# Performance work log

Measured on AMD Instinct MI355X. Metric: run time of the kernel, lower is better.

## Reference

```python
import jax, jax.numpy as jnp
import numpy as np

N = 50000      # nodes
E = 800000     # edges (before self-loops)
F_IN = 128     # raw node feature dim
D = 500        # GCN_in_dim = gcn_dim = h_mlp_dim
T = 200000     # number of triplets


def setup_inputs() -> dict:
    key = jax.random.key(0)
    ks = jax.random.split(key, 13)
    s = 0.05
    return {
        "feats": jax.random.normal(ks[0], (N, F_IN), jnp.float32),
        "W_aff": jax.random.normal(ks[1], (F_IN, D), jnp.float32) * s,
        "b_aff": jax.random.normal(ks[2], (D,), jnp.float32) * s,
        "W_gcn": jax.random.normal(ks[3], (D, D), jnp.float32) * s,
        "b_gcn": jax.random.normal(ks[4], (D,), jnp.float32) * s,
        "W_pred_in": jax.random.normal(ks[5], (2 * D, D), jnp.float32) * s,
        "b_pred_in": jax.random.normal(ks[6], (D,), jnp.float32) * s,
        "W_pred_out": jax.random.normal(ks[7], (D, 1), jnp.float32) * s,
        "b_pred_out": jax.random.normal(ks[8], (1,), jnp.float32) * s,
        "src": jax.random.randint(ks[9], (E,), 0, N),
        "dst": jax.random.randint(ks[10], (E,), 0, N),
        "triplets": jax.random.randint(ks[11], (T, 3), 0, N),
    }


def reference(feats, W_aff, b_aff, W_gcn, b_gcn, W_pred_in, b_pred_in,
              W_pred_out, b_pred_out, src, dst, triplets):
    n = feats.shape[0]
    # LinearAffine (use_pre_linearAffine=True)
    x = feats @ W_aff + b_aff                      # [N, D]

    # dgl.add_self_loop
    loop = jnp.arange(n)
    s_idx = jnp.concatenate([src, loop])
    d_idx = jnp.concatenate([dst, loop])

    # GraphConv, norm='both', no edge weights, activation=None
    ones = jnp.ones(s_idx.shape[0], jnp.float32)
    out_deg = jax.ops.segment_sum(ones, s_idx, num_segments=n)
    in_deg = jax.ops.segment_sum(ones, d_idx, num_segments=n)
    norm_src = jnp.where(out_deg > 0, jax.lax.rsqrt(out_deg), 0.0)  # [N]
    norm_dst = jnp.where(in_deg > 0, jax.lax.rsqrt(in_deg), 0.0)    # [N]

    xw = x @ W_gcn                                  # [N, D]
    msg = xw[s_idx] * norm_src[s_idx, None]         # [E+N, D] gather
    agg = jax.ops.segment_sum(msg, d_idx, num_segments=n)  # scatter-add
    embedding = agg * norm_dst[:, None] + b_gcn     # [N, D]

    # triplet gather + MLP_edge_predictor (layer_num=2: cat->Linear->Linear)
    s_feat = embedding[triplets[:, 0]]              # [T, D]
    o_feat = embedding[triplets[:, 2]]              # [T, D]
    t = jnp.concatenate([s_feat, o_feat], axis=-1) @ W_pred_in + b_pred_in
    weights = t @ W_pred_out + b_pred_out           # [T, 1]
    return (weights, embedding)
```

## Files before the change

### kernel.cpp

```cpp
#include <hip/hip_runtime.h>


typedef float f32x4 __attribute__((ext_vector_type(4)));
typedef short s16x8 __attribute__((ext_vector_type(8)));

__device__ __forceinline__ unsigned short f2bf(float f) {
    unsigned u = __float_as_uint(f);
    unsigned r = (u + 0x7FFFu + ((u >> 16) & 1u)) >> 16;
    return (unsigned short)r;
}

__device__ __forceinline__ void async_ld16(const void* g, void* lds) {
    __builtin_amdgcn_global_load_lds(
        (const __attribute__((address_space(1))) unsigned int*)g,
        (__attribute__((address_space(3))) unsigned int*)lds,
        16, 0, 0);
}

__global__ __launch_bounds__(256) void init_kernel(
    float* __restrict__ u, int nU4, unsigned* __restrict__ gpad, int nG,
    float* __restrict__ hpad, int nH, int* __restrict__ bh, int nB) {
    const int stride = gridDim.x * blockDim.x;
    const int i0 = blockIdx.x * blockDim.x + threadIdx.x;
    for (int i = i0; i < nU4; i += stride)
        *reinterpret_cast<float4*>(u + i * 4) = make_float4(0.f, 0.f, 0.f, 0.f);
    for (int i = i0; i < nG; i += stride) gpad[i] = 0u;
    for (int i = i0; i < nH; i += stride) hpad[i] = 0.f;
    for (int i = i0; i < nB; i += stride) bh[i] = 0;
}

__global__ __launch_bounds__(256) void hist2_kernel(
    const int* __restrict__ src, const int* __restrict__ dst,
    int* __restrict__ bhist_src, int* __restrict__ bhist_dst, int E) {
    __shared__ int lhs[256], lhd[256];
    lhs[threadIdx.x] = 0;
    lhd[threadIdx.x] = 0;
    __syncthreads();
    const int stride = gridDim.x * blockDim.x;
    for (int e = blockIdx.x * blockDim.x + threadIdx.x; e < E; e += stride) {
        atomicAdd(&lhs[src[e] >> 8], 1);
        atomicAdd(&lhd[dst[e] >> 8], 1);
    }
    __syncthreads();
    int cs = lhs[threadIdx.x], cd = lhd[threadIdx.x];
    if (cs > 0) atomicAdd(&bhist_src[threadIdx.x], cs);
    if (cd > 0) atomicAdd(&bhist_dst[threadIdx.x], cd);
}

__global__ void bscan2_kernel(const int* __restrict__ bhist_src, const int* __restrict__ bhist_dst,
                              int* __restrict__ sbbase, int* __restrict__ sbcursor,
                              int* __restrict__ dbbase, int* __restrict__ dbcursor,
                              int nbuk, int E) {
    __shared__ int sv[256];
    const int tid = threadIdx.x;

    int c = (tid < nbuk) ? bhist_src[tid] : 0;
    sv[tid] = c;
    __syncthreads();
    for (int st = 1; st < 256; st <<= 1) {
        int t = (tid >= st) ? sv[tid - st] : 0;
        __syncthreads();
        sv[tid] += t;
        __syncthreads();
    }
    if (tid < nbuk) { int ex = sv[tid] - c; sbbase[tid] = ex; sbcursor[tid] = ex; }
    if (tid == 0) sbbase[nbuk] = E;
    __syncthreads();

    c = (tid < nbuk) ? bhist_dst[tid] : 0;
    sv[tid] = c;
    __syncthreads();
    for (int st = 1; st < 256; st <<= 1) {
        int t = (tid >= st) ? sv[tid - st] : 0;
        __syncthreads();
        sv[tid] += t;
        __syncthreads();
    }
    if (tid < nbuk) { int ex = sv[tid] - c; dbbase[tid] = ex; dbcursor[tid] = ex; }
    if (tid == 0) dbbase[nbuk] = E;
}

#define PCH 4096
__global__ __launch_bounds__(256) void fused_partition_kernel(
    const int* __restrict__ src, const int* __restrict__ dst,
    int* __restrict__ dcursor, unsigned long long* __restrict__ pairs,
    int* __restrict__ scursor, int* __restrict__ ssorted,
    int E, int nbuk) {
    __shared__ int lhist[256];
    __shared__ int lbase[256];
    __shared__ int gbase[256];
    __shared__ int scanv[256];
    __shared__ unsigned long long lpair[PCH];
    __shared__ unsigned char lbid[PCH];

    const int tid = threadIdx.x;
    const int c0 = blockIdx.x * PCH;
    int cnt = E - c0; if (cnt > PCH) cnt = PCH;

    int dv[16], sv[16], rk[16];

    lhist[tid] = 0;
    __syncthreads();
#pragma unroll
    for (int q = 0; q < 16; ++q) {
        int e = c0 + q * 256 + tid;
        if (e < E) {
            int d = dst[e];
            dv[q] = d;
            sv[q] = src[e];
            rk[q] = atomicAdd(&lhist[d >> 8], 1);
        } else {
            dv[q] = -1;
            sv[q] = -1;
        }
    }
    __syncthreads();

    int c = lhist[tid];
    scanv[tid] = c;
    __syncthreads();
    for (int st = 1; st < 256; st <<= 1) {
        int t = (tid >= st) ? scanv[tid - st] : 0;
        __syncthreads();
        scanv[tid] += t;
        __syncthreads();
    }
    lbase[tid] = scanv[tid] - c;
    if (tid < nbuk && c > 0) gbase[tid] = atomicAdd(&dcursor[tid], c);
    __syncthreads();

#pragma unroll
    for (int q = 0; q < 16; ++q) {
        if (dv[q] >= 0) {
            int b = dv[q] >> 8;
            int slot = lbase[b] + rk[q];
            lpair[slot] = ((unsigned long long)(unsigned)dv[q] << 32) | (unsigned)sv[q];
            lbid[slot] = (unsigned char)b;
        }
    }
    __syncthreads();

    for (int i = tid; i < cnt; i += 256) {
        int b = lbid[i];
        pairs[(long)gbase[b] + (i - lbase[b])] = lpair[i];
    }
    __syncthreads();

    int* lval = (int*)lpair;
    lhist[tid] = 0;
    __syncthreads();
#pragma unroll
    for (int q = 0; q < 16; ++q) {
        if (sv[q] >= 0) rk[q] = atomicAdd(&lhist[sv[q] >> 8], 1);
    }
    __syncthreads();

    c = lhist[tid];
    scanv[tid] = c;
    __syncthreads();
    for (int st = 1; st < 256; st <<= 1) {
        int t = (tid >= st) ? scanv[tid - st] : 0;
        __syncthreads();
        scanv[tid] += t;
        __syncthreads();
    }
    lbase[tid] = scanv[tid] - c;
    if (tid < nbuk && c > 0) gbase[tid] = atomicAdd(&scursor[tid], c);
    __syncthreads();

#pragma unroll
    for (int q = 0; q < 16; ++q) {
        if (sv[q] >= 0) {
            int b = sv[q] >> 8;
            int slot = lbase[b] + rk[q];
            lval[slot] = sv[q];
            lbid[slot] = (unsigned char)b;
        }
    }
    __syncthreads();

    for (int i = tid; i < cnt; i += 256) {
        int b = lbid[i];
        ssorted[(long)gbase[b] + (i - lbase[b])] = lval[i];
    }
}

__global__ __launch_bounds__(256) void bucket_finalize_kernel(
    const unsigned long long* __restrict__ pairs, const int* __restrict__ dbbase,
    const int* __restrict__ ssorted, const int* __restrict__ sbbase,
    const float* __restrict__ feats,
    int* __restrict__ row_ptr, float* __restrict__ ndv,
    int* __restrict__ csr_src, float* __restrict__ ns,
    unsigned short* __restrict__ fs16, int N) {
    __shared__ int hist[256];
    __shared__ int scanv[256];
    __shared__ int lcur[256];
    __shared__ float nsv[256];
    const int tid = threadIdx.x;
    const int b = blockIdx.x;
    const int node = b * 256 + tid;

    const int e0 = dbbase[b], e1 = dbbase[b + 1];
    hist[tid] = 0;
    __syncthreads();
    for (int e = e0 + tid; e < e1; e += 256) {
        int d = (int)(pairs[e] >> 32);
        atomicAdd(&hist[d & 255], 1);
    }
    __syncthreads();

    int c = hist[tid];
    scanv[tid] = c;
    __syncthreads();
    for (int st = 1; st < 256; st <<= 1) {
        int t = (tid >= st) ? scanv[tid - st] : 0;
        __syncthreads();
        scanv[tid] += t;
        __syncthreads();
    }
    int excl = scanv[tid] - c;
    if (node < N) {
        row_ptr[node] = e0 + excl;
        ndv[node] = rsqrtf((float)(c + 1));
    }
    if (node == N) row_ptr[N] = e0 + excl;
    lcur[tid] = excl;
    __syncthreads();

    for (int e = e0 + tid; e < e1; e += 256) {
        unsigned long long pr = pairs[e];
        int d = (int)(pr >> 32);
        int r = atomicAdd(&lcur[d & 255], 1);
        csr_src[e0 + r] = (int)(pr & 0xFFFFFFFFu);
    }

    __syncthreads();
    hist[tid] = 0;
    __syncthreads();
    const int s0 = sbbase[b], s1 = sbbase[b + 1];
    for (int e = s0 + tid; e < s1; e += 256) atomicAdd(&hist[ssorted[e] & 255], 1);
    __syncthreads();
    float nsval = rsqrtf((float)(hist[tid] + 1));
    nsv[tid] = nsval;
    if (node < N) ns[node] = nsval;
    __syncthreads();

    for (int r0 = 0; r0 < 256; r0 += 16) {
        int r = r0 + (tid >> 4);
        int nn = b * 256 + r;
        if (nn >= N) break;
        int cq = (tid & 15) * 8;
        float s = nsv[r];
        const float* pf = feats + (long)nn * 128 + cq;
        float4 a = *reinterpret_cast<const float4*>(pf);
        float4 d2 = *reinterpret_cast<const float4*>(pf + 4);
        uint4 o;
        o.x = (unsigned)f2bf(a.x * s) | ((unsigned)f2bf(a.y * s) << 16);
        o.y = (unsigned)f2bf(a.z * s) | ((unsigned)f2bf(a.w * s) << 16);
        o.z = (unsigned)f2bf(d2.x * s) | ((unsigned)f2bf(d2.y * s) << 16);
        o.w = (unsigned)f2bf(d2.z * s) | ((unsigned)f2bf(d2.w * s) << 16);
        *reinterpret_cast<uint4*>(fs16 + (long)nn * 128 + cq) = o;
    }
}

__global__ __launch_bounds__(256) void prep1_kernel(
    const float* __restrict__ b_aff, const float* __restrict__ W_gcn,
    float* __restrict__ part,
    const float* __restrict__ Win, const float* __restrict__ wout,
    float* __restrict__ v,
    const float* __restrict__ b_in, const float* __restrict__ b_out,
    float* __restrict__ bdot,
    int D, int PD, int NBbc, int NBv, int nbper) {
    __shared__ float sm[256];
    const int b = blockIdx.x;
    const int tid = threadIdx.x;

    if (b < NBbc) {
        int nblk = b % nbper;
        int cch = b / nbper;
        int n = nblk * 256 + tid;
        if (n >= PD) return;
        float s = 0.f;
        if (n < D) {
            int k0 = cch * 8;
            int k1 = k0 + 8; if (k1 > D) k1 = D;
            for (int k = k0; k < k1; ++k) s = fmaf(b_aff[k], W_gcn[(long)k * D + n], s);
        }
        part[(long)cch * PD + n] = s;
    } else if (b < NBbc + NBv) {
        int k = (b - NBbc) * 4 + (tid >> 6);
        int lane = tid & 63;
        if (k >= 2 * D) return;
        float s = 0.f;
        for (int cc = lane; cc < D; cc += 64) s = fmaf(Win[(long)k * D + cc], wout[cc], s);
#pragma unroll
        for (int m = 32; m > 0; m >>= 1) s += __shfl_down(s, m);
        if (lane == 0) v[k] = s;
    } else {
        float s = 0.f;
        for (int cc = tid; cc < D; cc += 256) s = fmaf(b_in[cc], wout[cc], s);
        sm[tid] = s;
        __syncthreads();
        for (int st = 128; st > 0; st >>= 1) {
            if (tid < st) sm[tid] += sm[tid + st];
            __syncthreads();
        }
        if (tid == 0) bdot[0] = sm[0] + b_out[0];
    }
}

__global__ __launch_bounds__(256) void sgemm_kernel(const float* __restrict__ A, int lda,
                                                    const float* __restrict__ B, int ldb,
                                                    float* __restrict__ Cp, int ldc,
                                                    int M, int N, int K) {
    __shared__ __align__(16) float As[16][68];
    __shared__ __align__(16) float Bs[16][68];
    const int tid = threadIdx.x;
    const int tx = tid & 15, ty = tid >> 4;
    const int row0 = blockIdx.x * 64;
    const int col0 = blockIdx.y * 64;
    const int kbeg = blockIdx.z * 128;
    int kend = kbeg + 128; if (kend > K) kend = K;
    float* C = Cp + (long)blockIdx.z * M * ldc;

    const int a_row = tid >> 2;
    const int a_k   = (tid & 3) * 4;
    const int b_k   = tid >> 4;
    const int b_c   = (tid & 15) * 4;

    float acc[4][4] = {};

    for (int k0 = kbeg; k0 < kend; k0 += 16) {
        float4 av = make_float4(0.f, 0.f, 0.f, 0.f);
        {
            int gr = row0 + a_row;
            int gk = k0 + a_k;
            if (gr < M) {
                if (gk + 3 < kend) {
                    av = *reinterpret_cast<const float4*>(&A[(long)gr * lda + gk]);
                } else {
                    float t0 = (gk + 0 < kend) ? A[(long)gr * lda + gk + 0] : 0.f;
                    float t1 = (gk + 1 < kend) ? A[(long)gr * lda + gk + 1] : 0.f;
                    float t2 = (gk + 2 < kend) ? A[(long)gr * lda + gk + 2] : 0.f;
                    float t3 = (gk + 3 < kend) ? A[(long)gr * lda + gk + 3] : 0.f;
                    av = make_float4(t0, t1, t2, t3);
                }
            }
        }
        float4 bv = make_float4(0.f, 0.f, 0.f, 0.f);
        {
            int gk = k0 + b_k;
            int gc = col0 + b_c;
            if (gk < kend) {
                if (gc + 3 < N) {
                    bv = *reinterpret_cast<const float4*>(&B[(long)gk * ldb + gc]);
                } else {
                    float t0 = (gc + 0 < N) ? B[(long)gk * ldb + gc + 0] : 0.f;
                    float t1 = (gc + 1 < N) ? B[(long)gk * ldb + gc + 1] : 0.f;
                    float t2 = (gc + 2 < N) ? B[(long)gk * ldb + gc + 2] : 0.f;
                    float t3 = (gc + 3 < N) ? B[(long)gk * ldb + gc + 3] : 0.f;
                    bv = make_float4(t0, t1, t2, t3);
                }
            }
        }
        __syncthreads();
        As[a_k + 0][a_row] = av.x;
        As[a_k + 1][a_row] = av.y;
        As[a_k + 2][a_row] = av.z;
        As[a_k + 3][a_row] = av.w;
        *reinterpret_cast<float4*>(&Bs[b_k][b_c]) = bv;
        __syncthreads();

#pragma unroll
        for (int k = 0; k < 16; ++k) {
            const float4 a = *reinterpret_cast<const float4*>(&As[k][ty * 4]);
            const float4 b = *reinterpret_cast<const float4*>(&Bs[k][tx * 4]);
            const float avv[4] = {a.x, a.y, a.z, a.w};
            const float bvv[4] = {b.x, b.y, b.z, b.w};
#pragma unroll
            for (int i = 0; i < 4; ++i)
#pragma unroll
                for (int j = 0; j < 4; ++j)
                    acc[i][j] = fmaf(avv[i], bvv[j], acc[i][j]);
        }
    }

#pragma unroll
    for (int i = 0; i < 4; ++i) {
        int r = row0 + ty * 4 + i;
        if (r >= M) continue;
#pragma unroll
        for (int j = 0; j < 4; ++j) {
            int c = col0 + tx * 4 + j;
            if (c < N) C[(long)r * ldc + c] = acc[i][j];
        }
    }
}

__global__ __launch_bounds__(256) void convBt_pad_kernel(
    const float* __restrict__ Wcp, unsigned short* __restrict__ Bt,
    const float* __restrict__ part, const float* __restrict__ b_gcn,
    const float* __restrict__ v, float* __restrict__ bcp,
    float* __restrict__ bgp, float* __restrict__ v1p, float* __restrict__ v2p,
    int D, int PD, int NC, int F, int nConvBlk) {
    const int b = blockIdx.x;
    const int tid = threadIdx.x;
    if (b < nConvBlk) {
        int idx = b * 256 + tid;
        if (idx >= PD * 16) return;
        int n = idx >> 4;
        int k8 = (idx & 15) * 8;
        uint4 o = make_uint4(0, 0, 0, 0);
        if (n < D) {
            unsigned short t[8];
            const long FD = (long)F * D;
#pragma unroll
            for (int q = 0; q < 8; ++q) {
                long off = (long)(k8 + q) * D + n;
                float val = Wcp[off] + Wcp[FD + off] + Wcp[2 * FD + off] + Wcp[3 * FD + off];
                t[q] = f2bf(val);
            }
            o.x = (unsigned)t[0] | ((unsigned)t[1] << 16);
            o.y = (unsigned)t[2] | ((unsigned)t[3] << 16);
            o.z = (unsigned)t[4] | ((unsigned)t[5] << 16);
            o.w = (unsigned)t[6] | ((unsigned)t[7] << 16);
        }
        *reinterpret_cast<uint4*>(Bt + (long)n * 128 + k8) = o;
    } else {
        int i = (b - nConvBlk) * 256 + tid;
        if (i < PD) {
            float s = 0.f;
            for (int c = 0; c < NC; ++c) s += part[(long)c * PD + i];
            bcp[i] = s;
            bgp[i] = (i < D) ? b_gcn[i] : 0.f;
            v1p[i] = (i < D) ? v[i] : 0.f;
            v2p[i] = (i < D) ? v[D + i] : 0.f;
        }
    }
}

__global__ __launch_bounds__(256) void gather_feats_kernel(
    const unsigned short* __restrict__ fs16, const int* __restrict__ csr_src,
    const int* __restrict__ row_ptr, const float* __restrict__ ns,
    unsigned short* __restrict__ g16, float* __restrict__ h, int N) {
    int d = blockIdx.x * 4 + (threadIdx.x >> 6);
    int lane = threadIdx.x & 63;
    if (d >= N) return;
    const int g = lane >> 4;
    const int fl = lane & 15;

    float a[8] = {0.f, 0.f, 0.f, 0.f, 0.f, 0.f, 0.f, 0.f};
    float hacc = 0.f;

    const int beg = row_ptr[d], end = row_ptr[d + 1];
    for (int j0 = beg; j0 < end; j0 += 64) {
        int cnt = end - j0;
        if (cnt > 64) cnt = 64;
        int s = (lane < cnt) ? csr_src[j0 + lane] : 0;
        if (lane < cnt) hacc += ns[s];
        for (int k = 0; k < cnt; k += 8) {
            int k0 = k + g, k1 = k + 4 + g;
            int i0 = __shfl(s, k0 & 63);
            int i1 = __shfl(s, k1 & 63);
            uint4 v0 = make_uint4(0u, 0u, 0u, 0u), v1 = make_uint4(0u, 0u, 0u, 0u);
            if (k0 < cnt) v0 = *reinterpret_cast<const uint4*>(fs16 + (long)i0 * 128 + fl * 8);
            if (k1 < cnt) v1 = *reinterpret_cast<const uint4*>(fs16 + (long)i1 * 128 + fl * 8);
            a[0] += __uint_as_float(v0.x << 16); a[1] += __uint_as_float(v0.x & 0xFFFF0000u);
            a[2] += __uint_as_float(v0.y << 16); a[3] += __uint_as_float(v0.y & 0xFFFF0000u);
            a[4] += __uint_as_float(v0.z << 16); a[5] += __uint_as_float(v0.z & 0xFFFF0000u);
            a[6] += __uint_as_float(v0.w << 16); a[7] += __uint_as_float(v0.w & 0xFFFF0000u);
            a[0] += __uint_as_float(v1.x << 16); a[1] += __uint_as_float(v1.x & 0xFFFF0000u);
            a[2] += __uint_as_float(v1.y << 16); a[3] += __uint_as_float(v1.y & 0xFFFF0000u);
            a[4] += __uint_as_float(v1.z << 16); a[5] += __uint_as_float(v1.z & 0xFFFF0000u);
            a[6] += __uint_as_float(v1.w << 16); a[7] += __uint_as_float(v1.w & 0xFFFF0000u);
        }
    }

#pragma unroll
    for (int r = 0; r < 8; ++r) {
        a[r] += __shfl_xor(a[r], 16);
        a[r] += __shfl_xor(a[r], 32);
    }
    {
        uint4 sv4 = *reinterpret_cast<const uint4*>(fs16 + (long)d * 128 + fl * 8);
        a[0] += __uint_as_float(sv4.x << 16); a[1] += __uint_as_float(sv4.x & 0xFFFF0000u);
        a[2] += __uint_as_float(sv4.y << 16); a[3] += __uint_as_float(sv4.y & 0xFFFF0000u);
        a[4] += __uint_as_float(sv4.z << 16); a[5] += __uint_as_float(sv4.z & 0xFFFF0000u);
        a[6] += __uint_as_float(sv4.w << 16); a[7] += __uint_as_float(sv4.w & 0xFFFF0000u);
    }
#pragma unroll
    for (int m = 32; m > 0; m >>= 1) hacc += __shfl_xor(hacc, m);
    if (lane == 0) h[d] = hacc + ns[d];
    if (lane < 16) {
        uint4 o;
        o.x = (unsigned)f2bf(a[0]) | ((unsigned)f2bf(a[1]) << 16);
        o.y = (unsigned)f2bf(a[2]) | ((unsigned)f2bf(a[3]) << 16);
        o.z = (unsigned)f2bf(a[4]) | ((unsigned)f2bf(a[5]) << 16);
        o.w = (unsigned)f2bf(a[6]) | ((unsigned)f2bf(a[7]) << 16);
        *reinterpret_cast<uint4*>(g16 + (long)d * 128 + fl * 8) = o;
    }
}

__global__ __launch_bounds__(256) void gcn_gemm_kernel(
    const unsigned short* __restrict__ g16, const unsigned short* __restrict__ Bt,
    const float* __restrict__ h, const float* __restrict__ nd,
    const float* __restrict__ bcp, const float* __restrict__ bgp,
    const float* __restrict__ v1p, const float* __restrict__ v2p,
    float* __restrict__ emb, float* __restrict__ u1, float* __restrict__ u2,
    int M, int D) {

    __shared__ __align__(16) unsigned short As[128 * 32];
    __shared__ __align__(16) unsigned short Bs[128 * 32];

    const int tid  = threadIdx.x;
    const int w    = tid >> 6;
    const int lane = tid & 63;
    const int row0 = blockIdx.x * 128;
    const int col0 = blockIdx.y * 128;

    const int r0   = 2 * w * 16 + (lane >> 2);
    const int r1   = (2 * w + 1) * 16 + (lane >> 2);
    const int slot = lane & 3;
    const int c0   = slot ^ ((r0 >> 1) & 3);
    const int c1   = slot ^ ((r1 >> 1) & 3);

    const unsigned short* pA0 = g16 + (long)(row0 + r0) * 128 + c0 * 8;
    const unsigned short* pA1 = g16 + (long)(row0 + r1) * 128 + c1 * 8;
    const unsigned short* pB0 = Bt + (long)(col0 + r0) * 128 + c0 * 8;
    const unsigned short* pB1 = Bt + (long)(col0 + r1) * 128 + c1 * 8;

    unsigned short* dA0 = As + 2 * w * 512;
    unsigned short* dA1 = As + (2 * w + 1) * 512;
    unsigned short* dB0 = Bs + 2 * w * 512;
    unsigned short* dB1 = Bs + (2 * w + 1) * 512;

    const int wrow = (w & 1) * 64;
    const int wcol = (w >> 1) * 64;
    const int lm = lane & 15, q = lane >> 4;
    const s16x8* pa[4];
    const s16x8* pb[4];
#pragma unroll
    for (int i = 0; i < 4; ++i) {
        int r = wrow + i * 16 + lm;
        int cs = q ^ ((r >> 1) & 3);
        pa[i] = reinterpret_cast<const s16x8*>(As + r * 32 + cs * 8);
        int n = wcol + i * 16 + lm;
        int cs2 = q ^ ((n >> 1) & 3);
        pb[i] = reinterpret_cast<const s16x8*>(Bs + n * 32 + cs2 * 8);
    }

    f32x4 acc[4][4];
#pragma unroll
    for (int i = 0; i < 4; ++i)
#pragma unroll
        for (int j = 0; j < 4; ++j) acc[i][j] = (f32x4)0.f;

    for (int k0 = 0; k0 < 128; k0 += 32) {
        async_ld16(pA0 + k0, dA0);
        async_ld16(pA1 + k0, dA1);
        async_ld16(pB0 + k0, dB0);
        async_ld16(pB1 + k0, dB1);
        __syncthreads();

        s16x8 af[4], bf[4];
#pragma unroll
        for (int i = 0; i < 4; ++i) { af[i] = *pa[i]; bf[i] = *pb[i]; }
#pragma unroll
        for (int i = 0; i < 4; ++i)
#pragma unroll
            for (int j = 0; j < 4; ++j)
                acc[i][j] = __builtin_amdgcn_mfma_f32_16x16x32_bf16(af[i], bf[j], acc[i][j], 0, 0, 0);
        __syncthreads();
    }

    float bcv[4], bgv[4], w1[4], w2[4];
    int colv[4];
#pragma unroll
    for (int j = 0; j < 4; ++j) {
        int c = col0 + wcol + j * 16 + lm;
        colv[j] = c;
        bcv[j] = bcp[c];
        bgv[j] = bgp[c];
        w1[j] = v1p[c];
        w2[j] = v2p[c];
    }

#pragma unroll
    for (int i = 0; i < 4; ++i) {
        float p1[4], p2[4];
#pragma unroll
        for (int reg = 0; reg < 4; ++reg) {
            int row = row0 + wrow + i * 16 + q * 4 + reg;
            float hb = h[row];
            float sc = nd[row];
            float s1 = 0.f, s2 = 0.f;
#pragma unroll
            for (int j = 0; j < 4; ++j) {
                float o = fmaf(sc, acc[i][j][reg] + hb * bcv[j], bgv[j]);
                if (row < M && colv[j] < D) emb[(long)row * D + colv[j]] = o;
                s1 = fmaf(o, w1[j], s1);
                s2 = fmaf(o, w2[j], s2);
            }
            p1[reg] = s1;
            p2[reg] = s2;
        }
#pragma unroll
        for (int mask = 1; mask < 16; mask <<= 1)
#pragma unroll
            for (int reg = 0; reg < 4; ++reg) {
                p1[reg] += __shfl_xor(p1[reg], mask);
                p2[reg] += __shfl_xor(p2[reg], mask);
            }
        if (lm == 0) {
#pragma unroll
            for (int reg = 0; reg < 4; ++reg) {
                int row = row0 + wrow + i * 16 + q * 4 + reg;
                if (row < M) {
                    atomicAdd(&u1[row], p1[reg]);
                    atomicAdd(&u2[row], p2[reg]);
                }
            }
        }
    }
}

__global__ void weights_kernel(const int* __restrict__ trip, const float* __restrict__ u1,
                               const float* __restrict__ u2, const float* __restrict__ bdot,
                               float* __restrict__ w, int T) {
    int r = blockIdx.x * blockDim.x + threadIdx.x;
    if (r < T) {
        int s = trip[(long)r * 3 + 0];
        int o = trip[(long)r * 3 + 2];
        w[r] = u1[s] + u2[o] + bdot[0];
    }
}


extern "C" void kernel_launch(void* const* d_in, const int* in_sizes, int n_in,
                              void* d_out, int out_size, void* d_ws, size_t ws_size,
                              hipStream_t stream) {
    const float* feats      = (const float*)d_in[0];
    const float* W_aff      = (const float*)d_in[1];
    const float* b_aff      = (const float*)d_in[2];
    const float* W_gcn      = (const float*)d_in[3];
    const float* b_gcn      = (const float*)d_in[4];
    const float* W_pred_in  = (const float*)d_in[5];
    const float* b_pred_in  = (const float*)d_in[6];
    const float* W_pred_out = (const float*)d_in[7];
    const float* b_pred_out = (const float*)d_in[8];
    const int*   src        = (const int*)d_in[9];
    const int*   dst        = (const int*)d_in[10];
    const int*   trip       = (const int*)d_in[11];

    const int D = in_sizes[2];
    const int F = in_sizes[1] / D;
    const int N = in_sizes[0] / F;
    const int E = in_sizes[9];
    const int T = in_sizes[11] / 3;

    const int PD = 512;
    const int GX = (N + 127) / 128;
    const int Mpad = GX * 128;
    const int NC = (D + 7) / 8;
    const int NBUK = (N >> 8) + 1;
    const int KS = 4;

    float* weights = (float*)d_out;
    float* emb     = (float*)d_out + T;

    char* p = (char*)d_ws;
    unsigned short* fs16 = (unsigned short*)p;  p += (size_t)N * 128 * 2;
    unsigned short* g16  = (unsigned short*)p;  p += (size_t)Mpad * 128 * 2;
    unsigned long long* pairs = (unsigned long long*)p; p += (size_t)E * 8;
    int* ssorted = (int*)p;  p += (size_t)E * 4;
    unsigned short* Bt   = (unsigned short*)p;  p += (size_t)PD * 128 * 2;
    float* Wcp  = (float*)p;  p += (size_t)KS * F * D * 4;
    float* bparts = (float*)p;  p += (size_t)64 * PD * 4;
    float* bcp  = (float*)p;  p += PD * 4;
    float* bgp  = (float*)p;  p += PD * 4;
    float* v1p  = (float*)p;  p += PD * 4;
    float* v2p  = (float*)p;  p += PD * 4;
    float* v    = (float*)p;  p += 1024 * 4;
    float* bdot = (float*)p;  p += 16;
    float* ns   = (float*)p;  p += (size_t)N * 4;
    float* nd   = (float*)p;  p += (size_t)N * 4;
    float* h    = (float*)p;  p += (size_t)Mpad * 4;
    float* u1   = (float*)p;  p += (size_t)N * 4;
    float* u2   = (float*)p;  p += (size_t)N * 4;
    int* bhist_src = (int*)p;  p += 256 * 4;
    int* bhist_dst = (int*)p;  p += 256 * 4;
    int* sbbase   = (int*)p;  p += 260 * 4;
    int* sbcursor = (int*)p;  p += 256 * 4;
    int* dbbase   = (int*)p;  p += 260 * 4;
    int* dbcursor = (int*)p;  p += 256 * 4;
    int* row_ptr = (int*)p;  p += (size_t)(N + 1) * 4;
    int* csr_src = (int*)p;  p += (size_t)E * 4;

    init_kernel<<<128, 256, 0, stream>>>(
        u1, (2 * N) / 4,
        (unsigned*)(g16 + (size_t)N * 128), (Mpad - N) * 128 / 2,
        h + N, Mpad - N,
        bhist_src, 512);

    hist2_kernel<<<256, 256, 0, stream>>>(src, dst, bhist_src, bhist_dst, E);
    bscan2_kernel<<<1, 256, 0, stream>>>(bhist_src, bhist_dst, sbbase, sbcursor,
                                         dbbase, dbcursor, NBUK, E);
    fused_partition_kernel<<<(E + PCH - 1) / PCH, 256, 0, stream>>>(
        src, dst, dbcursor, pairs, sbcursor, ssorted, E, NBUK);
    bucket_finalize_kernel<<<NBUK, 256, 0, stream>>>(pairs, dbbase, ssorted, sbbase,
                                                     feats, row_ptr, nd, csr_src, ns,
                                                     fs16, N);

    {
        const int nbper = (PD + 255) / 256;
        const int NBbc = nbper * NC;
        const int NBv = (2 * D + 3) / 4;
        prep1_kernel<<<NBbc + NBv + 1, 256, 0, stream>>>(
            b_aff, W_gcn, bparts, W_pred_in, W_pred_out, v,
            b_pred_in, b_pred_out, bdot, D, PD, NBbc, NBv, nbper);
    }
    {
        dim3 grid((F + 63) / 64, (D + 63) / 64, KS);
        sgemm_kernel<<<grid, 256, 0, stream>>>(W_aff, D, W_gcn, D, Wcp, D, F, D, D);
    }
    {
        const int nConvBlk = (PD * 16 + 255) / 256;
        const int nPadBlk = (PD + 255) / 256;
        convBt_pad_kernel<<<nConvBlk + nPadBlk, 256, 0, stream>>>(
            Wcp, Bt, bparts, b_gcn, v, bcp, bgp, v1p, v2p, D, PD, NC, F, nConvBlk);
    }

    gather_feats_kernel<<<(N + 3) / 4, 256, 0, stream>>>(fs16, csr_src, row_ptr, ns, g16, h, N);

    {
        dim3 grid(GX, PD / 128);
        gcn_gemm_kernel<<<grid, 256, 0, stream>>>(g16, Bt, h, nd, bcp, bgp, v1p, v2p,
                                                  emb, u1, u2, N, D);
    }

    weights_kernel<<<(T + 255) / 256, 256, 0, stream>>>(trip, u1, u2, bdot, weights, T);
}
```

Before: 315.2 us.

## Loop all column tiles inside GCN GEMM block and fuse prep kernels

The GCN GEMM now launches one block per 128-row tile. The block loads the full 128x128 A tile into LDS once and loops over the four 128-column output tiles. The per-row u1/u2 dot products are reduced in LDS and written once, so the global atomics and the u1/u2 zero-init go away. The small sgemm and prep1 kernels are merged into a single launch. The cost is fewer blocks for the main GEMM (less parallelism) and more LDS per block, which may lower occupancy.

```diff
diff --git a/kernel.cpp b/kernel.cpp
--- a/kernel.cpp
+++ b/kernel.cpp
@@ -18,12 +18,10 @@
 }
 
 __global__ __launch_bounds__(256) void init_kernel(
-    float* __restrict__ u, int nU4, unsigned* __restrict__ gpad, int nG,
+    unsigned* __restrict__ gpad, int nG,
     float* __restrict__ hpad, int nH, int* __restrict__ bh, int nB) {
     const int stride = gridDim.x * blockDim.x;
     const int i0 = blockIdx.x * blockDim.x + threadIdx.x;
-    for (int i = i0; i < nU4; i += stride)
-        *reinterpret_cast<float4*>(u + i * 4) = make_float4(0.f, 0.f, 0.f, 0.f);
     for (int i = i0; i < nG; i += stride) gpad[i] = 0u;
     for (int i = i0; i < nH; i += stride) hpad[i] = 0.f;
     for (int i = i0; i < nB; i += stride) bh[i] = 0;
@@ -263,32 +261,119 @@
     }
 }
 
-__global__ __launch_bounds__(256) void prep1_kernel(
-    const float* __restrict__ b_aff, const float* __restrict__ W_gcn,
-    float* __restrict__ part,
+__global__ __launch_bounds__(256) void dense_prep_kernel(
+    const float* __restrict__ A, int lda,
+    const float* __restrict__ B, int ldb,
+    float* __restrict__ Cp, int ldc, int M, int Nn, int K,
+    const float* __restrict__ b_aff, float* __restrict__ part,
     const float* __restrict__ Win, const float* __restrict__ wout,
     float* __restrict__ v,
     const float* __restrict__ b_in, const float* __restrict__ b_out,
     float* __restrict__ bdot,
-    int D, int PD, int NBbc, int NBv, int nbper) {
-    __shared__ float sm[256];
-    const int b = blockIdx.x;
+    int D, int PD, int gxn, int gyn, int NBsg, int NBbc, int NBv, int nbper) {
+    __shared__ __align__(16) float As[16][68];
+    __shared__ __align__(16) float Bs[16][68];
+    const int blk = blockIdx.x;
     const int tid = threadIdx.x;
 
-    if (b < NBbc) {
-        int nblk = b % nbper;
-        int cch = b / nbper;
+    if (blk < NBsg) {
+        const int gx = blk % gxn;
+        const int gy = (blk / gxn) % gyn;
+        const int gz = blk / (gxn * gyn);
+        const int tx = tid & 15, ty = tid >> 4;
+        const int row0 = gx * 64;
+        const int col0 = gy * 64;
+        const int kbeg = gz * 128;
+        int kend = kbeg + 128; if (kend > K) kend = K;
+        float* C = Cp + (long)gz * M * ldc;
+
+        const int a_row = tid >> 2;
+        const int a_k   = (tid & 3) * 4;
+        const int b_k   = tid >> 4;
+        const int b_c   = (tid & 15) * 4;
+
+        float acc[4][4] = {};
+
+        for (int k0 = kbeg; k0 < kend; k0 += 16) {
+            float4 av = make_float4(0.f, 0.f, 0.f, 0.f);
+            {
+                int gr = row0 + a_row;
+                int gk = k0 + a_k;
+                if (gr < M) {
+                    if (gk + 3 < kend) {
+                        av = *reinterpret_cast<const float4*>(&A[(long)gr * lda + gk]);
+                    } else {
+                        float t0 = (gk + 0 < kend) ? A[(long)gr * lda + gk + 0] : 0.f;
+                        float t1 = (gk + 1 < kend) ? A[(long)gr * lda + gk + 1] : 0.f;
+                        float t2 = (gk + 2 < kend) ? A[(long)gr * lda + gk + 2] : 0.f;
+                        float t3 = (gk + 3 < kend) ? A[(long)gr * lda + gk + 3] : 0.f;
+                        av = make_float4(t0, t1, t2, t3);
+                    }
+                }
+            }
+            float4 bv = make_float4(0.f, 0.f, 0.f, 0.f);
+            {
+                int gk = k0 + b_k;
+                int gc = col0 + b_c;
+                if (gk < kend) {
+                    if (gc + 3 < Nn) {
+                        bv = *reinterpret_cast<const float4*>(&B[(long)gk * ldb + gc]);
+                    } else {
+                        float t0 = (gc + 0 < Nn) ? B[(long)gk * ldb + gc + 0] : 0.f;
+                        float t1 = (gc + 1 < Nn) ? B[(long)gk * ldb + gc + 1] : 0.f;
+                        float t2 = (gc + 2 < Nn) ? B[(long)gk * ldb + gc + 2] : 0.f;
+                        float t3 = (gc + 3 < Nn) ? B[(long)gk * ldb + gc + 3] : 0.f;
+                        bv = make_float4(t0, t1, t2, t3);
+                    }
+                }
+            }
+            __syncthreads();
+            As[a_k + 0][a_row] = av.x;
+            As[a_k + 1][a_row] = av.y;
+            As[a_k + 2][a_row] = av.z;
+            As[a_k + 3][a_row] = av.w;
+            *reinterpret_cast<float4*>(&Bs[b_k][b_c]) = bv;
+            __syncthreads();
+
+#pragma unroll
+            for (int k = 0; k < 16; ++k) {
+                const float4 a = *reinterpret_cast<const float4*>(&As[k][ty * 4]);
+                const float4 b2 = *reinterpret_cast<const float4*>(&Bs[k][tx * 4]);
+                const float avv[4] = {a.x, a.y, a.z, a.w};
+                const float bvv[4] = {b2.x, b2.y, b2.z, b2.w};
+#pragma unroll
+                for (int i = 0; i < 4; ++i)
+#pragma unroll
+                    for (int j = 0; j < 4; ++j)
+                        acc[i][j] = fmaf(avv[i], bvv[j], acc[i][j]);
+            }
+        }
+
+#pragma unroll
+        for (int i = 0; i < 4; ++i) {
+            int r = row0 + ty * 4 + i;
+            if (r >= M) continue;
+#pragma unroll
+            for (int j = 0; j < 4; ++j) {
+                int cc = col0 + tx * 4 + j;
+                if (cc < Nn) C[(long)r * ldc + cc] = acc[i][j];
+            }
+        }
+    } else if (blk < NBsg + NBbc) {
+        int b2 = blk - NBsg;
+        int nblk = b2 % nbper;
+        int cch = b2 / nbper;
         int n = nblk * 256 + tid;
         if (n >= PD) return;
         float s = 0.f;
         if (n < D) {
             int k0 = cch * 8;
             int k1 = k0 + 8; if (k1 > D) k1 = D;
-            for (int k = k0; k < k1; ++k) s = fmaf(b_aff[k], W_gcn[(long)k * D + n], s);
+            for (int k = k0; k < k1; ++k) s = fmaf(b_aff[k], B[(long)k * ldb + n], s);
         }
         part[(long)cch * PD + n] = s;
-    } else if (b < NBbc + NBv) {
-        int k = (b - NBbc) * 4 + (tid >> 6);
+    } else if (blk < NBsg + NBbc + NBv) {
+        int k = (blk - NBsg - NBbc) * 4 + (tid >> 6);
         int lane = tid & 63;
         if (k >= 2 * D) return;
         float s = 0.f;
@@ -297,6 +382,7 @@
         for (int m = 32; m > 0; m >>= 1) s += __shfl_down(s, m);
         if (lane == 0) v[k] = s;
     } else {
+        float* sm = &As[0][0];
         float s = 0.f;
         for (int cc = tid; cc < D; cc += 256) s = fmaf(b_in[cc], wout[cc], s);
         sm[tid] = s;
@@ -306,94 +392,6 @@
             __syncthreads();
         }
         if (tid == 0) bdot[0] = sm[0] + b_out[0];
-    }
-}
-
-__global__ __launch_bounds__(256) void sgemm_kernel(const float* __restrict__ A, int lda,
-                                                    const float* __restrict__ B, int ldb,
-                                                    float* __restrict__ Cp, int ldc,
-                                                    int M, int N, int K) {
-    __shared__ __align__(16) float As[16][68];
-    __shared__ __align__(16) float Bs[16][68];
-    const int tid = threadIdx.x;
-    const int tx = tid & 15, ty = tid >> 4;
-    const int row0 = blockIdx.x * 64;
-    const int col0 = blockIdx.y * 64;
-    const int kbeg = blockIdx.z * 128;
-    int kend = kbeg + 128; if (kend > K) kend = K;
-    float* C = Cp + (long)blockIdx.z * M * ldc;
-
-    const int a_row = tid >> 2;
-    const int a_k   = (tid & 3) * 4;
-    const int b_k   = tid >> 4;
-    const int b_c   = (tid & 15) * 4;
-
-    float acc[4][4] = {};
-
-    for (int k0 = kbeg; k0 < kend; k0 += 16) {
-        float4 av = make_float4(0.f, 0.f, 0.f, 0.f);
-        {
-            int gr = row0 + a_row;
-            int gk = k0 + a_k;
-            if (gr < M) {
-                if (gk + 3 < kend) {
-                    av = *reinterpret_cast<const float4*>(&A[(long)gr * lda + gk]);
-                } else {
-                    float t0 = (gk + 0 < kend) ? A[(long)gr * lda + gk + 0] : 0.f;
-                    float t1 = (gk + 1 < kend) ? A[(long)gr * lda + gk + 1] : 0.f;
-                    float t2 = (gk + 2 < kend) ? A[(long)gr * lda + gk + 2] : 0.f;
-                    float t3 = (gk + 3 < kend) ? A[(long)gr * lda + gk + 3] : 0.f;
-                    av = make_float4(t0, t1, t2, t3);
-                }
-            }
-        }
-        float4 bv = make_float4(0.f, 0.f, 0.f, 0.f);
-        {
-            int gk = k0 + b_k;
-            int gc = col0 + b_c;
-            if (gk < kend) {
-                if (gc + 3 < N) {
-                    bv = *reinterpret_cast<const float4*>(&B[(long)gk * ldb + gc]);
-                } else {
-                    float t0 = (gc + 0 < N) ? B[(long)gk * ldb + gc + 0] : 0.f;
-                    float t1 = (gc + 1 < N) ? B[(long)gk * ldb + gc + 1] : 0.f;
-                    float t2 = (gc + 2 < N) ? B[(long)gk * ldb + gc + 2] : 0.f;
-                    float t3 = (gc + 3 < N) ? B[(long)gk * ldb + gc + 3] : 0.f;
-                    bv = make_float4(t0, t1, t2, t3);
-                }
-            }
-        }
-        __syncthreads();
-        As[a_k + 0][a_row] = av.x;
-        As[a_k + 1][a_row] = av.y;
-        As[a_k + 2][a_row] = av.z;
-        As[a_k + 3][a_row] = av.w;
-        *reinterpret_cast<float4*>(&Bs[b_k][b_c]) = bv;
-        __syncthreads();
-
-#pragma unroll
-        for (int k = 0; k < 16; ++k) {
-            const float4 a = *reinterpret_cast<const float4*>(&As[k][ty * 4]);
-            const float4 b = *reinterpret_cast<const float4*>(&Bs[k][tx * 4]);
-            const float avv[4] = {a.x, a.y, a.z, a.w};
-            const float bvv[4] = {b.x, b.y, b.z, b.w};
-#pragma unroll
-            for (int i = 0; i < 4; ++i)
-#pragma unroll
-                for (int j = 0; j < 4; ++j)
-                    acc[i][j] = fmaf(avv[i], bvv[j], acc[i][j]);
-        }
-    }
-
-#pragma unroll
-    for (int i = 0; i < 4; ++i) {
-        int r = row0 + ty * 4 + i;
-        if (r >= M) continue;
-#pragma unroll
-        for (int j = 0; j < 4; ++j) {
-            int c = col0 + tx * 4 + j;
-            if (c < N) C[(long)r * ldc + c] = acc[i][j];
-        }
     }
 }
 
@@ -509,14 +507,14 @@
     float* __restrict__ emb, float* __restrict__ u1, float* __restrict__ u2,
     int M, int D) {
 
-    __shared__ __align__(16) unsigned short As[128 * 32];
+    __shared__ __align__(16) unsigned short As[128 * 128];
     __shared__ __align__(16) unsigned short Bs[128 * 32];
+    __shared__ float us1[128], us2[128];
 
     const int tid  = threadIdx.x;
     const int w    = tid >> 6;
     const int lane = tid & 63;
     const int row0 = blockIdx.x * 128;
-    const int col0 = blockIdx.y * 128;
 
     const int r0   = 2 * w * 16 + (lane >> 2);
     const int r1   = (2 * w + 1) * 16 + (lane >> 2);
@@ -526,100 +524,121 @@
 
     const unsigned short* pA0 = g16 + (long)(row0 + r0) * 128 + c0 * 8;
     const unsigned short* pA1 = g16 + (long)(row0 + r1) * 128 + c1 * 8;
-    const unsigned short* pB0 = Bt + (long)(col0 + r0) * 128 + c0 * 8;
-    const unsigned short* pB1 = Bt + (long)(col0 + r1) * 128 + c1 * 8;
 
     unsigned short* dA0 = As + 2 * w * 512;
     unsigned short* dA1 = As + (2 * w + 1) * 512;
     unsigned short* dB0 = Bs + 2 * w * 512;
     unsigned short* dB1 = Bs + (2 * w + 1) * 512;
 
+#pragma unroll
+    for (int kc = 0; kc < 4; ++kc) {
+        async_ld16(pA0 + kc * 32, dA0 + kc * 4096);
+        async_ld16(pA1 + kc * 32, dA1 + kc * 4096);
+    }
+
+    if (tid < 128) { us1[tid] = 0.f; us2[tid] = 0.f; }
+
     const int wrow = (w & 1) * 64;
     const int wcol = (w >> 1) * 64;
     const int lm = lane & 15, q = lane >> 4;
-    const s16x8* pa[4];
-    const s16x8* pb[4];
-#pragma unroll
-    for (int i = 0; i < 4; ++i) {
-        int r = wrow + i * 16 + lm;
-        int cs = q ^ ((r >> 1) & 3);
-        pa[i] = reinterpret_cast<const s16x8*>(As + r * 32 + cs * 8);
-        int n = wcol + i * 16 + lm;
-        int cs2 = q ^ ((n >> 1) & 3);
-        pb[i] = reinterpret_cast<const s16x8*>(Bs + n * 32 + cs2 * 8);
-    }
-
-    f32x4 acc[4][4];
+
+    float usum1[4][4], usum2[4][4];
 #pragma unroll
     for (int i = 0; i < 4; ++i)
 #pragma unroll
-        for (int j = 0; j < 4; ++j) acc[i][j] = (f32x4)0.f;
-
-    for (int k0 = 0; k0 < 128; k0 += 32) {
-        async_ld16(pA0 + k0, dA0);
-        async_ld16(pA1 + k0, dA1);
-        async_ld16(pB0 + k0, dB0);
-        async_ld16(pB1 + k0, dB1);
-        __syncthreads();
-
-        s16x8 af[4], bf[4];
-#pragma unroll
-        for (int i = 0; i < 4; ++i) { af[i] = *pa[i]; bf[i] = *pb[i]; }
+        for (int r = 0; r < 4; ++r) { usum1[i][r] = 0.f; usum2[i][r] = 0.f; }
+
+    for (int ct = 0; ct < 4; ++ct) {
+        const int col0 = ct * 128;
+        const unsigned short* pB0 = Bt + (long)(col0 + r0) * 128 + c0 * 8;
+        const unsigned short* pB1 = Bt + (long)(col0 + r1) * 128 + c1 * 8;
+
+        f32x4 acc[4][4];
 #pragma unroll
         for (int i = 0; i < 4; ++i)
 #pragma unroll
-            for (int j = 0; j < 4; ++j)
-                acc[i][j] = __builtin_amdgcn_mfma_f32_16x16x32_bf16(af[i], bf[j], acc[i][j], 0, 0, 0);
-        __syncthreads();
-    }
-
-    float bcv[4], bgv[4], w1[4], w2[4];
-    int colv[4];
-#pragma unroll
-    for (int j = 0; j < 4; ++j) {
-        int c = col0 + wcol + j * 16 + lm;
-        colv[j] = c;
-        bcv[j] = bcp[c];
-        bgv[j] = bgp[c];
-        w1[j] = v1p[c];
-        w2[j] = v2p[c];
-    }
-
-#pragma unroll
-    for (int i = 0; i < 4; ++i) {
-        float p1[4], p2[4];
-#pragma unroll
-        for (int reg = 0; reg < 4; ++reg) {
-            int row = row0 + wrow + i * 16 + q * 4 + reg;
-            float hb = h[row];
-            float sc = nd[row];
-            float s1 = 0.f, s2 = 0.f;
-#pragma unroll
-            for (int j = 0; j < 4; ++j) {
-                float o = fmaf(sc, acc[i][j][reg] + hb * bcv[j], bgv[j]);
-                if (row < M && colv[j] < D) emb[(long)row * D + colv[j]] = o;
-                s1 = fmaf(o, w1[j], s1);
-                s2 = fmaf(o, w2[j], s2);
-            }
-            p1[reg] = s1;
-            p2[reg] = s2;
-        }
-#pragma unroll
-        for (int mask = 1; mask < 16; mask <<= 1)
-#pragma unroll
-            for (int reg = 0; reg < 4; ++reg) {
-                p1[reg] += __shfl_xor(p1[reg], mask);
-                p2[reg] += __shfl_xor(p2[reg], mask);
-            }
-        if (lm == 0) {
+            for (int j = 0; j < 4; ++j) acc[i][j] = (f32x4)0.f;
+
+        for (int kc = 0; kc < 4; ++kc) {
+            async_ld16(pB0 + kc * 32, dB0);
+            async_ld16(pB1 + kc * 32, dB1);
+            __syncthreads();
+
+            s16x8 af[4], bf[4];
+#pragma unroll
+            for (int i = 0; i < 4; ++i) {
+                int r = wrow + i * 16 + lm;
+                int cs = q ^ ((r >> 1) & 3);
+                af[i] = *reinterpret_cast<const s16x8*>(As + kc * 4096 + r * 32 + cs * 8);
+                int n = wcol + i * 16 + lm;
+                int cs2 = q ^ ((n >> 1) & 3);
+                bf[i] = *reinterpret_cast<const s16x8*>(Bs + n * 32 + cs2 * 8);
+            }
+#pragma unroll
+            for (int i = 0; i < 4; ++i)
+#pragma unroll
+                for (int j = 0; j < 4; ++j)
+                    acc[i][j] = __builtin_amdgcn_mfma_f32_16x16x32_bf16(af[i], bf[j], acc[i][j], 0, 0, 0);
+            __syncthreads();
+        }
+
+        float bcv[4], bgv[4], w1v[4], w2v[4];
+        int colv[4];
+#pragma unroll
+        for (int j = 0; j < 4; ++j) {
+            int cc = col0 + wcol + j * 16 + lm;
+            colv[j] = cc;
+            bcv[j] = bcp[cc];
+            bgv[j] = bgp[cc];
+            w1v[j] = v1p[cc];
+            w2v[j] = v2p[cc];
+        }
+#pragma unroll
+        for (int i = 0; i < 4; ++i) {
 #pragma unroll
             for (int reg = 0; reg < 4; ++reg) {
                 int row = row0 + wrow + i * 16 + q * 4 + reg;
-                if (row < M) {
-                    atomicAdd(&u1[row], p1[reg]);
-                    atomicAdd(&u2[row], p2[reg]);
+                float hb = h[row];
+                float sc = (row < M) ? nd[row] : 0.f;
+                float s1 = 0.f, s2 = 0.f;
+#pragma unroll
+                for (int j = 0; j < 4; ++j) {
+                    float o = fmaf(sc, acc[i][j][reg] + hb * bcv[j], bgv[j]);
+                    if (row < M && colv[j] < D) emb[(long)row * D + colv[j]] = o;
+                    s1 = fmaf(o, w1v[j], s1);
+                    s2 = fmaf(o, w2v[j], s2);
                 }
-            }
+                usum1[i][reg] += s1;
+                usum2[i][reg] += s2;
+            }
+        }
+    }
+
+#pragma unroll
+    for (int mask = 1; mask < 16; mask <<= 1)
+#pragma unroll
+        for (int i = 0; i < 4; ++i)
+#pragma unroll
+            for (int reg = 0; reg < 4; ++reg) {
+                usum1[i][reg] += __shfl_xor(usum1[i][reg], mask);
+                usum2[i][reg] += __shfl_xor(usum2[i][reg], mask);
+            }
+    if (lm == 0) {
+#pragma unroll
+        for (int i = 0; i < 4; ++i)
+#pragma unroll
+            for (int reg = 0; reg < 4; ++reg) {
+                int lr = wrow + i * 16 + q * 4 + reg;
+                atomicAdd(&us1[lr], usum1[i][reg]);
+                atomicAdd(&us2[lr], usum2[i][reg]);
+            }
+    }
+    __syncthreads();
+    if (tid < 128) {
+        int row = row0 + tid;
+        if (row < M) {
+            u1[row] = us1[tid];
+            u2[row] = us2[tid];
         }
     }
 }
@@ -697,7 +716,6 @@
     int* csr_src = (int*)p;  p += (size_t)E * 4;
 
     init_kernel<<<128, 256, 0, stream>>>(
-        u1, (2 * N) / 4,
         (unsigned*)(g16 + (size_t)N * 128), (Mpad - N) * 128 / 2,
         h + N, Mpad - N,
         bhist_src, 512);
@@ -712,16 +730,17 @@
                                                      fs16, N);
 
     {
+        const int gxn = (F + 63) / 64;
+        const int gyn = (D + 63) / 64;
+        const int NBsg = gxn * gyn * KS;
         const int nbper = (PD + 255) / 256;
         const int NBbc = nbper * NC;
         const int NBv = (2 * D + 3) / 4;
-        prep1_kernel<<<NBbc + NBv + 1, 256, 0, stream>>>(
-            b_aff, W_gcn, bparts, W_pred_in, W_pred_out, v,
-            b_pred_in, b_pred_out, bdot, D, PD, NBbc, NBv, nbper);
-    }
-    {
-        dim3 grid((F + 63) / 64, (D + 63) / 64, KS);
-        sgemm_kernel<<<grid, 256, 0, stream>>>(W_aff, D, W_gcn, D, Wcp, D, F, D, D);
+        dense_prep_kernel<<<NBsg + NBbc + NBv + 1, 256, 0, stream>>>(
+            W_aff, D, W_gcn, D, Wcp, D, F, D, D,
+            b_aff, bparts, W_pred_in, W_pred_out, v,
+            b_pred_in, b_pred_out, bdot,
+            D, PD, gxn, gyn, NBsg, NBbc, NBv, nbper);
     }
     {
         const int nConvBlk = (PD * 16 + 255) / 256;
@@ -732,11 +751,8 @@
 
     gather_feats_kernel<<<(N + 3) / 4, 256, 0, stream>>>(fs16, csr_src, row_ptr, ns, g16, h, N);
 
-    {
-        dim3 grid(GX, PD / 128);
-        gcn_gemm_kernel<<<grid, 256, 0, stream>>>(g16, Bt, h, nd, bcp, bgp, v1p, v2p,
-                                                  emb, u1, u2, N, D);
-    }
+    gcn_gemm_kernel<<<GX, 256, 0, stream>>>(g16, Bt, h, nd, bcp, bgp, v1p, v2p,
+                                            emb, u1, u2, N, D);
 
     weights_kernel<<<(T + 255) / 256, 256, 0, stream>>>(trip, u1, u2, bdot, weights, T);
 }
```

Result: no change. 316.2 us (+0.3%).
